# Kernel optimization log

Measured on AMD Instinct MI355X. Metric: run time of the kernel, lower is better.

The kernel has to match this reference:

```python
import jax, jax.numpy as jnp
import numpy as np

EPS = 1e-5
SLOPE = 0.01  # torch LeakyReLU default

def _conv(x, w, b, stride):
    # x: [B,C,L], w: [O,I,3]
    y = jax.lax.conv_general_dilated(x, w, (stride,), [(1, 1)],
                                     dimension_numbers=("NCH", "OIH", "NCH"))
    return y + b[None, :, None]

def _bn(x, g, b, m, v):
    # eval-mode BatchNorm1d with running stats
    inv = jax.lax.rsqrt(v + EPS)
    return (x - m[None, :, None]) * (g * inv)[None, :, None] + b[None, :, None]

def _lrelu(x):
    return jnp.where(x >= 0, x, SLOPE * x)

def setup_inputs() -> dict:
    key = jax.random.key(0)
    ks = jax.random.split(key, 32)
    B, C, L = 32, 256, 2048
    K, D = 4096, 128
    d = {}
    d["x"] = jax.random.normal(ks[0], (B, C, L), dtype=jnp.float32)
    # conv weights [O,I,3]
    d["w1"] = jax.random.normal(ks[1], (256, 256, 3), jnp.float32) * 0.03
    d["b1"] = jax.random.normal(ks[2], (256,), jnp.float32) * 0.01
    d["w2"] = jax.random.normal(ks[3], (512, 256, 3), jnp.float32) * 0.03
    d["b2"] = jax.random.normal(ks[4], (512,), jnp.float32) * 0.01
    d["w3"] = jax.random.normal(ks[5], (512, 512, 3), jnp.float32) * 0.02
    d["b3"] = jax.random.normal(ks[6], (512,), jnp.float32) * 0.01
    d["w4"] = jax.random.normal(ks[7], (D, 512, 3), jnp.float32) * 0.02
    d["b4"] = jax.random.normal(ks[8], (D,), jnp.float32) * 0.01
    for i, ch in enumerate([256, 512, 512, D]):
        d[f"g{i+1}"] = 1.0 + 0.1 * jax.random.normal(ks[9 + 4 * i], (ch,), jnp.float32)
        d[f"be{i+1}"] = 0.1 * jax.random.normal(ks[10 + 4 * i], (ch,), jnp.float32)
        d[f"m{i+1}"] = 0.1 * jax.random.normal(ks[11 + 4 * i], (ch,), jnp.float32)
        d[f"v{i+1}"] = 0.5 + jax.random.uniform(ks[12 + 4 * i], (ch,), jnp.float32)
    d["emb"] = jax.random.uniform(ks[30], (K, D), jnp.float32,
                                  minval=-1.0 / K, maxval=1.0 / K)
    return d

def reference(x, w1, b1, w2, b2, w3, b3, w4, b4,
              g1, be1, m1, v1, g2, be2, m2, v2,
              g3, be3, m3, v3, g4, be4, m4, v4, emb):
    h = _lrelu(_bn(_conv(x, w1, b1, 2), g1, be1, m1, v1))   # [B,256,L/2]
    h = _lrelu(_bn(_conv(h, w2, b2, 2), g2, be2, m2, v2))   # [B,512,L/4]
    h = _lrelu(_bn(_conv(h, w3, b3, 2), g3, be3, m3, v3))   # [B,512,L/8]
    h = _lrelu(_bn(_conv(h, w4, b4, 1), g4, be4, m4, v4))   # [B,D,L/8]
    flat = jnp.transpose(h, (0, 2, 1)).reshape(-1, h.shape[1])  # [N,D]
    # squared-distance expansion: ||f||^2 + ||e||^2 - 2 f.e
    dist = (jnp.sum(flat * flat, axis=1, keepdims=True)
            + jnp.sum(emb * emb, axis=1)
            - 2.0 * flat @ emb.T)                            # [N,K]
    codes = jnp.argmin(dist, axis=1)
    return codes, dist
```

## Files before the change

### kernel.cpp

```cpp
#include <hip/hip_runtime.h>
#include <cstdint>
#include <math.h>

#define EPS_BN 1e-5f
#define SLOPE 0.01f
#define C14 6.103515625e-5f
#define SC14 16384.0f
#define HMIN 6.103515625e-5f

typedef __attribute__((ext_vector_type(8))) _Float16 half8;
typedef __attribute__((ext_vector_type(8))) short short8;
typedef __attribute__((ext_vector_type(16))) float f32x16;
typedef __attribute__((ext_vector_type(4))) float f32x4;

__device__ __forceinline__ void split16(float v, unsigned short& uh,
                                        unsigned short& ul) {
    _Float16 h = (_Float16)v;
    if (fabsf(v) < HMIN) h = (_Float16)0.0f;
    float rem = v - (float)h;
    _Float16 l = (_Float16)(rem * SC14);
    uh = __builtin_bit_cast(unsigned short, h);
    ul = __builtin_bit_cast(unsigned short, l);
}

typedef const __attribute__((address_space(1))) unsigned int* gas_ptr;
typedef __attribute__((address_space(3))) unsigned int* las_ptr;
__device__ __forceinline__ void glds16(const void* g, void* l) {
    __builtin_amdgcn_global_load_lds((gas_ptr)g, (las_ptr)l, 16, 0, 0);
}

__global__ __launch_bounds__(256)
void wprep_all(const float* __restrict__ w1, short* __restrict__ o1,
               const float* __restrict__ w2, short* __restrict__ o2,
               const float* __restrict__ w3, short* __restrict__ o3,
               const float* __restrict__ w4, short* __restrict__ o4)
{
    const float* w; short* wbuf; int CIN, COUT;
    switch (blockIdx.y) {
        case 0: w = w1; wbuf = o1; CIN = 256; COUT = 256; break;
        case 1: w = w2; wbuf = o2; CIN = 256; COUT = 512; break;
        case 2: w = w3; wbuf = o3; CIN = 512; COUT = 512; break;
        default: w = w4; wbuf = o4; CIN = 512; COUT = 128; break;
    }
    int KST = CIN / 16, OB = COUT / 128;
    int total = KST * OB * 1536;
    for (int sid = blockIdx.x * 256 + threadIdx.x; sid < total;
         sid += gridDim.x * 256) {
        int slot = sid % 1536;
        int kb = sid / 1536;
        int ob = kb % OB, ks = kb / OB;
        int m = slot & 31, hi = (slot >> 5) & 1, mf = (slot >> 6) & 3;
        int ts = slot >> 8;
        int t = ts >> 1, s = ts & 1;
        int oc = ob * 128 + mf * 32 + m;
        int ib = ks * 16 + hi * 8;
        short8 r;
        #pragma unroll
        for (int j = 0; j < 8; ++j) {
            float v = w[((size_t)oc * CIN + ib + j) * 3 + t];
            unsigned short uh, ul;
            split16(v, uh, ul);
            r[j] = (short)(s == 0 ? uh : ul);
        }
        *(short8*)(wbuf + (size_t)sid * 8) = r;
    }
}

__global__ __launch_bounds__(256)
void bnprep_init(
    const float* __restrict__ g1, const float* __restrict__ be1,
    const float* __restrict__ m1, const float* __restrict__ v1,
    const float* __restrict__ b1, float* __restrict__ sc1, float* __restrict__ off1,
    const float* __restrict__ g2, const float* __restrict__ be2,
    const float* __restrict__ m2, const float* __restrict__ v2,
    const float* __restrict__ b2, float* __restrict__ sc2, float* __restrict__ off2,
    const float* __restrict__ g3, const float* __restrict__ be3,
    const float* __restrict__ m3, const float* __restrict__ v3,
    const float* __restrict__ b3, float* __restrict__ sc3, float* __restrict__ off3,
    const float* __restrict__ g4, const float* __restrict__ be4,
    const float* __restrict__ m4, const float* __restrict__ v4,
    const float* __restrict__ b4, float* __restrict__ sc4, float* __restrict__ off4,
    unsigned long long* __restrict__ mp)
{
    int bid = blockIdx.x;
    if (bid >= 6) {
        mp[(bid - 6) * 256 + threadIdx.x] = ~0ULL;
        return;
    }
    const float *g, *be, *m, *v, *bias;
    float *sc, *off;
    int c;
    if (bid == 0) {
        g = g1; be = be1; m = m1; v = v1; bias = b1; sc = sc1; off = off1;
        c = threadIdx.x;
    } else if (bid <= 2) {
        g = g2; be = be2; m = m2; v = v2; bias = b2; sc = sc2; off = off2;
        c = (bid - 1) * 256 + threadIdx.x;
    } else if (bid <= 4) {
        g = g3; be = be3; m = m3; v = v3; bias = b3; sc = sc3; off = off3;
        c = (bid - 3) * 256 + threadIdx.x;
    } else {
        g = g4; be = be4; m = m4; v = v4; bias = b4; sc = sc4; off = off4;
        c = threadIdx.x;
        if (c >= 128) return;
    }
    float s = g[c] / sqrtf(v[c] + EPS_BN);
    sc[c] = s;
    off[c] = (bias[c] - m[c]) * s + be[c];
}

__global__ __launch_bounds__(256)
void xsplit(const float* __restrict__ x, short* __restrict__ xpl)
{
    const size_t PL = (size_t)32 * 32 * 2 * 1025 * 8;
    int l = blockIdx.x * 256 + threadIdx.x;
    int g = blockIdx.y, b = blockIdx.z;
    float v[8];
    #pragma unroll
    for (int j = 0; j < 8; ++j)
        v[j] = x[((size_t)b * 256 + g * 8 + j) * 2048 + l];
    int arr = l & 1;
    int slot = arr ? (l + 1) / 2 : l / 2 + 1;
    size_t base = ((((size_t)b * 32 + g) * 2 + arr) * 1025 + slot) * 8;
    short8 rh, rl;
    #pragma unroll
    for (int j = 0; j < 8; ++j) {
        unsigned short uh, ul;
        split16(v[j], uh, ul);
        rh[j] = (short)uh; rl[j] = (short)ul;
    }
    *(short8*)(xpl + base) = rh;
    *(short8*)(xpl + PL + base) = rl;
    if (l == 0) {
        short8 z;
        #pragma unroll
        for (int j = 0; j < 8; ++j) z[j] = 0;
        for (int sg = 0; sg < 2; ++sg)
            for (int a2 = 0; a2 < 2; ++a2)
                *(short8*)(xpl + sg * PL +
                           ((((size_t)b * 32 + g) * 2 + a2) * 1025) * 8) = z;
    }
}

template<int CIN, int COUT, int LIN, int TILE, int EPI>
__global__ __launch_bounds__(512, 1)
void conv_pair(const short* __restrict__ wbuf, const short* __restrict__ xpl,
               const float* __restrict__ scv, const float* __restrict__ offv,
               short* __restrict__ opl)
{
    constexpr int LOUT = LIN / 2;
    constexpr int KST = CIN / 16;
    constexpr int OBS = COUT / 128;
    constexpr int NG = CIN / 8;
    constexpr int SLOTS = LIN / 2 + 1;
    constexpr size_t PLIN = (size_t)32 * NG * 2 * SLOTS * 8;
    constexpr int NF = TILE / 64;
    constexpr int NGo = COUT / 8;
    constexpr int OSLOTS = (EPI == 0) ? (LOUT / 2 + 1) : (LOUT + 2);
    constexpr size_t PLOUT = (size_t)32 * NGo * ((EPI == 0) ? 2 : 1) * OSLOTS * 8;

    constexpr int XOFF = 49152;
    constexpr int SCOFF = 69632;
    __shared__ __align__(16) char lds[71680];

    const int tid = threadIdx.x;
    const int lane = tid & 63;
    const int wv = tid >> 6;
    const int wo = wv >> 2;
    const int wm = (wv >> 1) & 1, wn = wv & 1;
    const int hi = lane >> 5, n32 = lane & 31;
    const int n0 = blockIdx.x * TILE;
    const int oby = blockIdx.y;
    const int o0 = oby * 256;
    const int b = blockIdx.z;

    if (tid < 256) ((float*)(lds + SCOFF))[tid] = scv[o0 + tid];
    else ((float*)(lds + SCOFF + 1024))[tid - 256] = offv[o0 + tid - 256];

    f32x16 acc0[2][2], acc1[2][2];
    #pragma unroll
    for (int i = 0; i < 2; ++i)
        #pragma unroll
        for (int j = 0; j < 2; ++j)
            #pragma unroll
            for (int e = 0; e < 16; ++e) { acc0[i][j][e] = 0.0f; acc1[i][j][e] = 0.0f; }

    #pragma unroll 1
    for (int ks = 0; ks < KST; ++ks) {
        __syncthreads();
        {
            const short* wsrc = wbuf +
                ((size_t)ks * OBS + (oby * 2 + wo)) * 1536 * 8;
            #pragma unroll
            for (int it = 0; it < 6; ++it) {
                int slot0 = it * 256 + (wv & 3) * 64;
                glds16(wsrc + (size_t)(slot0 + lane) * 8,
                       lds + wo * 24576 + slot0 * 16);
            }
        }
        {
            int g0 = ks * 2;
            int r = wv;
            int sg = r >> 2, rhi = (r >> 1) & 1, arr = r & 1;
            int start = arr ? n0 : (n0 + 1);
            int cnt = arr ? (TILE + 1) : TILE;
            const short* src = xpl + (size_t)sg * PLIN
                + ((((size_t)b * NG + (g0 + rhi)) * 2 + arr) * SLOTS + start) * 8;
            char* dst = lds + XOFF + ((sg * 2 + rhi) * 2 + arr) * 2112;
            for (int c0 = 0; c0 < cnt; c0 += 64) {
                if (lane < cnt - c0)
                    glds16(src + (size_t)(c0 + lane) * 8, dst + c0 * 16);
            }
        }
        __syncthreads();
        #pragma unroll
        for (int t = 0; t < 3; ++t) {
            half8 af[2][2], bx[2][2];
            #pragma unroll
            for (int s = 0; s < 2; ++s) {
                #pragma unroll
                for (int mf = 0; mf < 2; ++mf)
                    af[s][mf] = *(const half8*)(lds + wo * 24576 +
                        (((t * 2 + s) * 4 + (wm * 2 + mf)) * 64 + lane) * 16);
                int arr = (t == 1) ? 0 : 1;
                int tof = (t == 2) ? 1 : 0;
                #pragma unroll
                for (int nf = 0; nf < NF; ++nf) {
                    int qb = wn * (TILE / 2) + nf * 32 + tof;
                    bx[s][nf] = *(const half8*)(lds + XOFF + s * 8448
                                                + arr * 2112 + qb * 16
                                                + hi * 4224 + n32 * 16);
                }
            }
            #pragma unroll
            for (int mf = 0; mf < 2; ++mf)
                #pragma unroll
                for (int nf = 0; nf < NF; ++nf) {
                    acc0[mf][nf] = __builtin_amdgcn_mfma_f32_32x32x16_f16(
                        af[0][mf], bx[0][nf], acc0[mf][nf], 0, 0, 0);
                    acc1[mf][nf] = __builtin_amdgcn_mfma_f32_32x32x16_f16(
                        af[0][mf], bx[1][nf], acc1[mf][nf], 0, 0, 0);
                    acc1[mf][nf] = __builtin_amdgcn_mfma_f32_32x32x16_f16(
                        af[1][mf], bx[0][nf], acc1[mf][nf], 0, 0, 0);
                }
        }
    }

    #pragma unroll
    for (int half = 0; half < NF; ++half) {
        __syncthreads();
        #pragma unroll
        for (int mf = 0; mf < 2; ++mf)
            #pragma unroll
            for (int r = 0; r < 16; ++r) {
                int ocl = mf * 32 + (r & 3) + 8 * (r >> 2) + 4 * hi;
                *(float*)(lds + wv * 8704 + n32 * 272 + ocl * 4) =
                    acc0[mf][half][r] + C14 * acc1[mf][half][r];
            }
        __syncthreads();
        #pragma unroll
        for (int it = 0; it < 4; ++it) {
            int sl = tid + it * 512;
            int w = sl >> 8, rem = sl & 255, p = rem >> 3, grp = rem & 7;
            int wo_ = w >> 2, wm_ = (w >> 1) & 1, wn_ = w & 1;
            f32x4 v0 = *(f32x4*)(lds + w * 8704 + p * 272 + grp * 32);
            f32x4 v1 = *(f32x4*)(lds + w * 8704 + p * 272 + grp * 32 + 16);
            int ocb = wo_ * 128 + wm_ * 64 + grp * 8;
            f32x4 s0 = *(f32x4*)(lds + SCOFF + ocb * 4);
            f32x4 s1 = *(f32x4*)(lds + SCOFF + ocb * 4 + 16);
            f32x4 q0 = *(f32x4*)(lds + SCOFF + 1024 + ocb * 4);
            f32x4 q1 = *(f32x4*)(lds + SCOFF + 1024 + ocb * 4 + 16);
            float y[8];
            #pragma unroll
            for (int j = 0; j < 4; ++j) {
                float a = v0[j] * s0[j] + q0[j];
                y[j] = a >= 0.0f ? a : SLOPE * a;
                float c = v1[j] * s1[j] + q1[j];
                y[4 + j] = c >= 0.0f ? c : SLOPE * c;
            }
            int pos_abs = n0 + wn_ * (TILE / 2) + half * 32 + p;
            int oc_abs = o0 + ocb;
            short8 rh, rl;
            #pragma unroll
            for (int j = 0; j < 8; ++j) {
                unsigned short uh, ul;
                split16(y[j], uh, ul);
                rh[j] = (short)uh; rl[j] = (short)ul;
            }
            int gq = oc_abs >> 3;
            size_t base;
            if (EPI == 0) {
                int arr = pos_abs & 1;
                int slot = arr ? (pos_abs + 1) / 2 : pos_abs / 2 + 1;
                base = ((((size_t)b * NGo + gq) * 2 + arr) * OSLOTS + slot) * 8;
            } else {
                base = (((size_t)b * NGo + gq) * OSLOTS + (pos_abs + 1)) * 8;
            }
            *(short8*)(opl + base) = rh;
            *(short8*)(opl + PLOUT + base) = rl;
        }
    }

    if (EPI == 0) {
        if (blockIdx.x == 0 && tid < 128) {
            int sg = tid >> 6, r2 = tid & 63, g16 = r2 >> 1, a2 = r2 & 1;
            int gq = oby * 32 + g16;
            short8 z;
            #pragma unroll
            for (int j = 0; j < 8; ++j) z[j] = 0;
            *(short8*)(opl + (size_t)sg * PLOUT +
                       ((((size_t)b * NGo + gq) * 2 + a2) * OSLOTS) * 8) = z;
        }
    } else {
        if (tid < 64 && (blockIdx.x == 0 || blockIdx.x == gridDim.x - 1)) {
            int sg = tid >> 5, g16 = tid & 31;
            int gq = oby * 32 + g16;
            int slot = (blockIdx.x == 0) ? 0 : (OSLOTS - 1);
            short8 z;
            #pragma unroll
            for (int j = 0; j < 8; ++j) z[j] = 0;
            *(short8*)(opl + (size_t)sg * PLOUT +
                       (((size_t)b * NGo + gq) * OSLOTS + slot) * 8) = z;
        }
    }
}

template<int CIN, int COUT, int LIN>
__global__ __launch_bounds__(256, 2)
void conv_s1(const short* __restrict__ wbuf, const short* __restrict__ xpl,
             const float* __restrict__ scv, const float* __restrict__ offv,
             float* __restrict__ fout)
{
    constexpr int KST = CIN / 16;
    constexpr int OB = COUT / 128;
    constexpr int NG = CIN / 8;
    constexpr int SLOTS = LIN + 2;
    constexpr size_t PLIN = (size_t)32 * NG * SLOTS * 8;

    constexpr int XOFF = 24576;
    constexpr int BUF  = 41472;
    constexpr int SCOFF = BUF;
    __shared__ __align__(16) char lds[BUF + 1024];

    const int tid = threadIdx.x;
    const int lane = tid & 63;
    const int wv = tid >> 6;
    const int wm = wv >> 1, wn = wv & 1;
    const int hi = lane >> 5, n32 = lane & 31;
    const int n0 = blockIdx.x * 128;
    const int ob = blockIdx.y;
    const int o0 = ob * 128;
    const int b = blockIdx.z;

    if (tid < 128) {
        ((float*)(lds + SCOFF))[tid] = scv[o0 + tid];
        ((float*)(lds + SCOFF + 512))[tid] = offv[o0 + tid];
    }

    f32x16 acc0[2][2], acc1[2][2];
    #pragma unroll
    for (int i = 0; i < 2; ++i)
        #pragma unroll
        for (int j = 0; j < 2; ++j)
            #pragma unroll
            for (int e = 0; e < 16; ++e) { acc0[i][j][e] = 0.0f; acc1[i][j][e] = 0.0f; }

    const short* wg = wbuf + (size_t)ob * 1536 * 8;
    const int lanexoff = hi * 4224 + n32 * 16;

    #pragma unroll 1
    for (int ks = 0; ks < KST; ++ks) {
        __syncthreads();
        {
            const short* wsrc = wg + (size_t)ks * OB * 1536 * 8;
            #pragma unroll
            for (int it = 0; it < 6; ++it) {
                int slot0 = it * 256 + wv * 64;
                glds16(wsrc + (size_t)(slot0 + lane) * 8, lds + slot0 * 16);
            }
        }
        {
            int g0 = ks * 2;
            for (int r = wv; r < 4; r += 4) {
                int sg = r >> 1, rhi = r & 1;
                const short* src = xpl + (size_t)sg * PLIN
                    + (((size_t)b * NG + (g0 + rhi)) * SLOTS + n0) * 8;
                char* dst = lds + XOFF + (sg * 2 + rhi) * 2112;
                for (int c0 = 0; c0 < 130; c0 += 64) {
                    if (lane < 130 - c0)
                        glds16(src + (size_t)(c0 + lane) * 8, dst + c0 * 16);
                }
            }
        }
        __syncthreads();
        #pragma unroll
        for (int t = 0; t < 3; ++t) {
            half8 af[2][2], bx[2][2];
            #pragma unroll
            for (int s = 0; s < 2; ++s) {
                #pragma unroll
                for (int mf = 0; mf < 2; ++mf)
                    af[s][mf] = *(const half8*)(lds +
                        (((t * 2 + s) * 4 + (wm * 2 + mf)) * 64 + lane) * 16);
                #pragma unroll
                for (int nf = 0; nf < 2; ++nf) {
                    int qb = wn * 64 + nf * 32 + t;
                    bx[s][nf] = *(const half8*)(lds + XOFF + s * 4224
                                                + qb * 16 + hi * 2112 + n32 * 16);
                }
            }
            #pragma unroll
            for (int mf = 0; mf < 2; ++mf)
                #pragma unroll
                for (int nf = 0; nf < 2; ++nf) {
                    acc0[mf][nf] = __builtin_amdgcn_mfma_f32_32x32x16_f16(
                        af[0][mf], bx[0][nf], acc0[mf][nf], 0, 0, 0);
                    acc1[mf][nf] = __builtin_amdgcn_mfma_f32_32x32x16_f16(
                        af[0][mf], bx[1][nf], acc1[mf][nf], 0, 0, 0);
                    acc1[mf][nf] = __builtin_amdgcn_mfma_f32_32x32x16_f16(
                        af[1][mf], bx[0][nf], acc1[mf][nf], 0, 0, 0);
                }
        }
    }

    #pragma unroll
    for (int half = 0; half < 2; ++half) {
        __syncthreads();
        #pragma unroll
        for (int mf = 0; mf < 2; ++mf)
            #pragma unroll
            for (int r = 0; r < 16; ++r) {
                int ocl = mf * 32 + (r & 3) + 8 * (r >> 2) + 4 * hi;
                *(float*)(lds + wv * 8704 + n32 * 272 + ocl * 4) =
                    acc0[mf][half][r] + C14 * acc1[mf][half][r];
            }
        __syncthreads();
        #pragma unroll
        for (int it = 0; it < 4; ++it) {
            int sl = tid + it * 256;
            int w = sl >> 8, rem = sl & 255, p = rem >> 3, grp = rem & 7;
            int wm_ = w >> 1, wn_ = w & 1;
            f32x4 v0 = *(f32x4*)(lds + w * 8704 + p * 272 + grp * 32);
            f32x4 v1 = *(f32x4*)(lds + w * 8704 + p * 272 + grp * 32 + 16);
            int oclb = wm_ * 64 + grp * 8;
            f32x4 s0 = *(f32x4*)(lds + SCOFF + oclb * 4);
            f32x4 s1 = *(f32x4*)(lds + SCOFF + oclb * 4 + 16);
            f32x4 q0 = *(f32x4*)(lds + SCOFF + 512 + oclb * 4);
            f32x4 q1 = *(f32x4*)(lds + SCOFF + 512 + oclb * 4 + 16);
            f32x4 w0, w1;
            #pragma unroll
            for (int j = 0; j < 4; ++j) {
                float a = v0[j] * s0[j] + q0[j];
                w0[j] = a >= 0.0f ? a : SLOPE * a;
                float c = v1[j] * s1[j] + q1[j];
                w1[j] = c >= 0.0f ? c : SLOPE * c;
            }
            int pos_abs = n0 + wn_ * 64 + half * 32 + p;
            float* fp = fout + ((size_t)(b * 256 + pos_abs)) * 128 + o0 + oclb;
            *(f32x4*)fp = w0;
            *(f32x4*)(fp + 4) = w1;
        }
    }
}

__global__ __launch_bounds__(256)
void split_kernel(const float* __restrict__ src, int nrows,
                  short* __restrict__ ph, short* __restrict__ pl,
                  float* __restrict__ sumv)
{
    int t = blockIdx.x * 256 + threadIdx.x;
    int n = t >> 4, g = t & 15;
    if (n >= nrows) return;
    const float* rowp = src + (size_t)n * 128 + g * 8;
    float4 v0 = *(const float4*)rowp;
    float4 v1 = *(const float4*)(rowp + 4);
    float vv[8] = {v0.x, v0.y, v0.z, v0.w, v1.x, v1.y, v1.z, v1.w};
    short8 rh, rl;
    float ss = 0.0f;
    #pragma unroll
    for (int j = 0; j < 8; ++j) {
        float v = vv[j];
        ss = fmaf(v, v, ss);
        unsigned short uh, ul;
        split16(v, uh, ul);
        rh[j] = (short)uh; rl[j] = (short)ul;
    }
    int nb = n >> 5, m = n & 31, ks = g >> 1, hi = g & 1;
    size_t slot = ((((size_t)nb * 8 + ks) * 2 + hi) * 32 + m) * 8;
    *(short8*)(ph + slot) = rh;
    *(short8*)(pl + slot) = rl;
    #pragma unroll
    for (int mk = 8; mk; mk >>= 1) ss += __shfl_xor(ss, mk);
    if (g == 0) sumv[n] = ss;
}

__global__ __launch_bounds__(256, 2)
void distmin_kernel(const short* __restrict__ fh, const short* __restrict__ fl,
                    const short* __restrict__ eh, const short* __restrict__ el,
                    const float* __restrict__ sf, const float* __restrict__ se,
                    float* __restrict__ dist, unsigned long long* __restrict__ mp)
{
    __shared__ unsigned long long cand[128 * 64];
    const int tid = threadIdx.x;
    const int lane = tid & 63;
    const int wv = tid >> 6;
    const int wm = wv >> 1, wn = wv & 1;
    const int hi = lane >> 5, n32 = lane & 31;
    const int kb = blockIdx.x;
    const int nb = blockIdx.y;

    f32x16 acc0[2][2], acc1[2][2];
    #pragma unroll
    for (int i = 0; i < 2; ++i)
        #pragma unroll
        for (int j = 0; j < 2; ++j)
            #pragma unroll
            for (int e = 0; e < 16; ++e) { acc0[i][j][e] = 0.0f; acc1[i][j][e] = 0.0f; }

    const short* fb[2][2];
    const short* eb[2][2];
    {
        const short* fpl[2] = {fh, fl};
        const short* epl[2] = {eh, el};
        #pragma unroll
        for (int s = 0; s < 2; ++s) {
            #pragma unroll
            for (int mf = 0; mf < 2; ++mf)
                fb[s][mf] = fpl[s] + (size_t)nb * 16384
                            + ((size_t)(wm * 2 + mf) * 8 * 64 + lane) * 8;
            #pragma unroll
            for (int nf = 0; nf < 2; ++nf)
                eb[s][nf] = epl[s]
                            + ((size_t)(kb * 4 + wn * 2 + nf) * 8 * 64 + lane) * 8;
        }
    }

    #pragma unroll
    for (int ks = 0; ks < 8; ++ks) {
        half8 af[2][2], bx[2][2];
        #pragma unroll
        for (int s = 0; s < 2; ++s) {
            #pragma unroll
            for (int mf = 0; mf < 2; ++mf)
                af[s][mf] = *(const half8*)(fb[s][mf] + ks * 512);
            #pragma unroll
            for (int nf = 0; nf < 2; ++nf)
                bx[s][nf] = *(const half8*)(eb[s][nf] + ks * 512);
        }
        #pragma unroll
        for (int mf = 0; mf < 2; ++mf)
            #pragma unroll
            for (int nf = 0; nf < 2; ++nf) {
                acc0[mf][nf] = __builtin_amdgcn_mfma_f32_32x32x16_f16(
                    af[0][mf], bx[0][nf], acc0[mf][nf], 0, 0, 0);
                acc1[mf][nf] = __builtin_amdgcn_mfma_f32_32x32x16_f16(
                    af[0][mf], bx[1][nf], acc1[mf][nf], 0, 0, 0);
                acc1[mf][nf] = __builtin_amdgcn_mfma_f32_32x32x16_f16(
                    af[1][mf], bx[0][nf], acc1[mf][nf], 0, 0, 0);
            }
    }

    const int n_blk = nb * 128;
    const int kc0 = kb * 128 + wn * 64 + n32;
    const float se0 = se[kc0];
    const float se1 = se[kc0 + 32];
    #pragma unroll
    for (int mf = 0; mf < 2; ++mf) {
        #pragma unroll
        for (int r = 0; r < 16; ++r) {
            int nloc = wm * 64 + mf * 32 + (r & 3) + 8 * (r >> 2) + 4 * hi;
            int n = n_blk + nloc;
            float sfn = sf[n];
            float d0 = acc0[mf][0][r] + C14 * acc1[mf][0][r];
            float d1 = acc0[mf][1][r] + C14 * acc1[mf][1][r];
            float v0 = (sfn + se0) - 2.0f * d0;
            float v1 = (sfn + se1) - 2.0f * d1;
            __builtin_nontemporal_store(v0, &dist[(size_t)n * 4096 + kc0]);
            __builtin_nontemporal_store(v1, &dist[(size_t)n * 4096 + kc0 + 32]);
            unsigned long long p0 =
                (((unsigned long long)__float_as_uint(v0)) << 32) | (unsigned)kc0;
            unsigned long long p1 =
                (((unsigned long long)__float_as_uint(v1)) << 32) | (unsigned)(kc0 + 32);
            unsigned long long p = p1 < p0 ? p1 : p0;
            cand[nloc * 64 + wn * 32 + n32] = p;
        }
    }
    __syncthreads();
    {
        int row = tid >> 1, h = tid & 1;
        unsigned long long best = ~0ULL;
        #pragma unroll
        for (int i = 0; i < 32; ++i) {
            int c = h * 32 + ((i + row) & 31);
            unsigned long long cv = cand[row * 64 + c];
            best = cv < best ? cv : best;
        }
        unsigned lo = (unsigned)best, hw = (unsigned)(best >> 32);
        unsigned lo2 = __shfl_xor(lo, 1), hw2 = __shfl_xor(hw, 1);
        unsigned long long ob = (((unsigned long long)hw2) << 32) | lo2;
        if (ob < best) best = ob;
        if (h == 0) atomicMin(mp + n_blk + row, best);
    }
}

__global__ __launch_bounds__(256)
void codes_kernel(const unsigned long long* __restrict__ mp,
                  float* __restrict__ codes)
{
    int n = blockIdx.x * 256 + threadIdx.x;
    if (n < 8192) codes[n] = (float)(unsigned)(mp[n] & 0xffffffffULL);
}

extern "C" void kernel_launch(void* const* d_in, const int* in_sizes, int n_in,
                              void* d_out, int out_size, void* d_ws, size_t ws_size,
                              hipStream_t stream)
{
    const float* x   = (const float*)d_in[0];
    const float* w1  = (const float*)d_in[1];
    const float* b1  = (const float*)d_in[2];
    const float* w2  = (const float*)d_in[3];
    const float* b2  = (const float*)d_in[4];
    const float* w3  = (const float*)d_in[5];
    const float* b3  = (const float*)d_in[6];
    const float* w4  = (const float*)d_in[7];
    const float* b4  = (const float*)d_in[8];
    const float* g1  = (const float*)d_in[9];
    const float* be1 = (const float*)d_in[10];
    const float* m1  = (const float*)d_in[11];
    const float* v1  = (const float*)d_in[12];
    const float* g2  = (const float*)d_in[13];
    const float* be2 = (const float*)d_in[14];
    const float* m2  = (const float*)d_in[15];
    const float* v2  = (const float*)d_in[16];
    const float* g3  = (const float*)d_in[17];
    const float* be3 = (const float*)d_in[18];
    const float* m3  = (const float*)d_in[19];
    const float* v3  = (const float*)d_in[20];
    const float* g4  = (const float*)d_in[21];
    const float* be4 = (const float*)d_in[22];
    const float* m4  = (const float*)d_in[23];
    const float* v4  = (const float*)d_in[24];
    const float* emb = (const float*)d_in[25];

    float* outf  = (float*)d_out;
    float* codes = outf;
    float* distm = outf + 8192;

    char* wsb = (char*)d_ws;
    short* wb1 = (short*)(wsb + 0);
    short* wb2 = (short*)(wsb + 786432);
    short* wb3 = (short*)(wsb + 2359296);
    short* wb4 = (short*)(wsb + 5505024);
    float* sc1 = (float*)(wsb + 6291456); float* off1 = sc1 + 256;
    float* sc2 = (float*)(wsb + 6293504); float* off2 = sc2 + 512;
    float* sc3 = (float*)(wsb + 6297600); float* off3 = sc3 + 512;
    float* sc4 = (float*)(wsb + 6301696); float* off4 = sc4 + 128;
    short* h1p = (short*)(wsb + 6302720);
    short* fh  = (short*)(wsb + 39922688);
    short* fl  = (short*)(wsb + 42019840);
    short* eh  = (short*)(wsb + 44116992);
    short* el  = (short*)(wsb + 45165568);
    float* sf  = (float*)(wsb + 46214144);
    float* se  = (float*)(wsb + 46246912);
    unsigned long long* mp = (unsigned long long*)(wsb + 46263296);

    char* db = (char*)distm;
    short* xpl = (short*)db;
    short* h2p = (short*)db;
    short* h3p = (short*)(db + 33685504);
    float* f   = (float*)(db + 80000000);

    wprep_all<<<dim3(192, 4), 256, 0, stream>>>(w1, wb1, w2, wb2, w3, wb3, w4, wb4);
    bnprep_init<<<38, 256, 0, stream>>>(
        g1, be1, m1, v1, b1, sc1, off1,
        g2, be2, m2, v2, b2, sc2, off2,
        g3, be3, m3, v3, b3, sc3, off3,
        g4, be4, m4, v4, b4, sc4, off4, mp);
    split_kernel<<<256, 256, 0, stream>>>(emb, 4096, eh, el, se);

    xsplit<<<dim3(8, 32, 32), 256, 0, stream>>>(x, xpl);
    conv_pair<256, 256, 2048, 128, 0>
        <<<dim3(8, 1, 32), 512, 0, stream>>>(wb1, xpl, sc1, off1, h1p);
    conv_pair<256, 512, 1024, 128, 0>
        <<<dim3(4, 2, 32), 512, 0, stream>>>(wb2, h1p, sc2, off2, h2p);
    conv_pair<512, 512, 512, 64, 1>
        <<<dim3(4, 2, 32), 512, 0, stream>>>(wb3, h2p, sc3, off3, h3p);
    conv_s1<512, 128, 256>
        <<<dim3(2, 1, 32), 256, 0, stream>>>(wb4, h3p, sc4, off4, f);

    split_kernel<<<512, 256, 0, stream>>>(f, 8192, fh, fl, sf);
    distmin_kernel<<<dim3(32, 64), 256, 0, stream>>>(fh, fl, eh, el,
                                                     sf, se, distm, mp);
    codes_kernel<<<32, 256, 0, stream>>>(mp, codes);
}
```

Before: 263.8 us.

## Double-buffer conv LDS staging and fuse feature split into final conv epilogue

Both conv kernels now keep two LDS buffers and issue the global-to-LDS loads for the next K step before computing the current one. They wait with explicit vmcnt counts and raw barriers, and raise wave priority around the MFMA block, so load latency overlaps compute. The last conv's epilogue now writes the fp16 hi/lo split features and atomically accumulates squared norms directly, removing the fp32 feature buffer and a separate split kernel launch. This costs twice the LDS per block and relies on hand-counted vmcnt values that must match the number of issued loads; the atomic norm accumulation also changes summation order.

```diff
diff --git a/kernel.cpp b/kernel.cpp
--- a/kernel.cpp
+++ b/kernel.cpp
@@ -27,6 +27,18 @@
 typedef __attribute__((address_space(3))) unsigned int* las_ptr;
 __device__ __forceinline__ void glds16(const void* g, void* l) {
     __builtin_amdgcn_global_load_lds((gas_ptr)g, (las_ptr)l, 16, 0, 0);
+}
+
+template<int N>
+__device__ __forceinline__ void vm_wait() {
+    if constexpr (N == 0)      asm volatile("s_waitcnt vmcnt(0)" ::: "memory");
+    else if constexpr (N == 8) asm volatile("s_waitcnt vmcnt(8)" ::: "memory");
+    else if constexpr (N == 9) asm volatile("s_waitcnt vmcnt(9)" ::: "memory");
+}
+__device__ __forceinline__ void raw_bar() {
+    asm volatile("" ::: "memory");
+    __builtin_amdgcn_s_barrier();
+    asm volatile("" ::: "memory");
 }
 
 __global__ __launch_bounds__(256)
@@ -80,13 +92,11 @@
     const float* __restrict__ g4, const float* __restrict__ be4,
     const float* __restrict__ m4, const float* __restrict__ v4,
     const float* __restrict__ b4, float* __restrict__ sc4, float* __restrict__ off4,
-    unsigned long long* __restrict__ mp)
+    unsigned long long* __restrict__ mp, float* __restrict__ sf)
 {
     int bid = blockIdx.x;
-    if (bid >= 6) {
-        mp[(bid - 6) * 256 + threadIdx.x] = ~0ULL;
-        return;
-    }
+    if (bid >= 38) { sf[(bid - 38) * 256 + threadIdx.x] = 0.0f; return; }
+    if (bid >= 6) { mp[(bid - 6) * 256 + threadIdx.x] = ~0ULL; return; }
     const float *g, *be, *m, *v, *bias;
     float *sc, *off;
     int c;
@@ -160,8 +170,10 @@
     constexpr size_t PLOUT = (size_t)32 * NGo * ((EPI == 0) ? 2 : 1) * OSLOTS * 8;
 
     constexpr int XOFF = 49152;
-    constexpr int SCOFF = 69632;
-    __shared__ __align__(16) char lds[71680];
+    constexpr int BUF  = XOFF + 8 * 2112;
+    constexpr int SCOFF = 2 * BUF;
+    constexpr int SCNT = (TILE == 128) ? 9 : 8;
+    __shared__ __align__(16) char lds[2 * BUF + 2048];
 
     const int tid = threadIdx.x;
     const int lane = tid & 63;
@@ -185,34 +197,45 @@
             #pragma unroll
             for (int e = 0; e < 16; ++e) { acc0[i][j][e] = 0.0f; acc1[i][j][e] = 0.0f; }
 
+    auto stage = [&](char* base, int ks) {
+        const short* wsrc = wbuf + ((size_t)ks * OBS + (oby * 2 + wo)) * 1536 * 8;
+        #pragma unroll
+        for (int it = 0; it < 6; ++it) {
+            int slot0 = it * 256 + (wv & 3) * 64;
+            glds16(wsrc + (size_t)(slot0 + lane) * 8, base + wo * 24576 + slot0 * 16);
+        }
+        int g0 = ks * 2;
+        int sg = wv >> 2, rhi = (wv >> 1) & 1, arr = wv & 1;
+        int start = arr ? n0 : (n0 + 1);
+        const short* src = xpl + (size_t)sg * PLIN
+            + ((((size_t)b * NG + (g0 + rhi)) * 2 + arr) * SLOTS + start) * 8;
+        char* dst = base + XOFF + ((sg * 2 + rhi) * 2 + arr) * 2112;
+        if (TILE == 128) {
+            glds16(src + (size_t)lane * 8, dst);
+            glds16(src + (size_t)(64 + lane) * 8, dst + 64 * 16);
+            int c2 = arr ? 65 : 64;
+            glds16(src + (size_t)(c2 + lane) * 8, dst + c2 * 16);
+        } else {
+            glds16(src + (size_t)lane * 8, dst);
+            int c1 = arr ? 1 : 0;
+            glds16(src + (size_t)(c1 + lane) * 8, dst + c1 * 16);
+        }
+    };
+
+    stage(lds, 0);
+
     #pragma unroll 1
     for (int ks = 0; ks < KST; ++ks) {
-        __syncthreads();
-        {
-            const short* wsrc = wbuf +
-                ((size_t)ks * OBS + (oby * 2 + wo)) * 1536 * 8;
-            #pragma unroll
-            for (int it = 0; it < 6; ++it) {
-                int slot0 = it * 256 + (wv & 3) * 64;
-                glds16(wsrc + (size_t)(slot0 + lane) * 8,
-                       lds + wo * 24576 + slot0 * 16);
-            }
-        }
-        {
-            int g0 = ks * 2;
-            int r = wv;
-            int sg = r >> 2, rhi = (r >> 1) & 1, arr = r & 1;
-            int start = arr ? n0 : (n0 + 1);
-            int cnt = arr ? (TILE + 1) : TILE;
-            const short* src = xpl + (size_t)sg * PLIN
-                + ((((size_t)b * NG + (g0 + rhi)) * 2 + arr) * SLOTS + start) * 8;
-            char* dst = lds + XOFF + ((sg * 2 + rhi) * 2 + arr) * 2112;
-            for (int c0 = 0; c0 < cnt; c0 += 64) {
-                if (lane < cnt - c0)
-                    glds16(src + (size_t)(c0 + lane) * 8, dst + c0 * 16);
-            }
-        }
-        __syncthreads();
+        char* cbase = lds + (ks & 1) * BUF;
+        char* nbase = lds + ((ks & 1) ^ 1) * BUF;
+        if (ks + 1 < KST) {
+            stage(nbase, ks + 1);
+            vm_wait<SCNT>();
+        } else {
+            vm_wait<0>();
+        }
+        raw_bar();
+        __builtin_amdgcn_s_setprio(1);
         #pragma unroll
         for (int t = 0; t < 3; ++t) {
             half8 af[2][2], bx[2][2];
@@ -220,14 +243,14 @@
             for (int s = 0; s < 2; ++s) {
                 #pragma unroll
                 for (int mf = 0; mf < 2; ++mf)
-                    af[s][mf] = *(const half8*)(lds + wo * 24576 +
+                    af[s][mf] = *(const half8*)(cbase + wo * 24576 +
                         (((t * 2 + s) * 4 + (wm * 2 + mf)) * 64 + lane) * 16);
                 int arr = (t == 1) ? 0 : 1;
                 int tof = (t == 2) ? 1 : 0;
                 #pragma unroll
                 for (int nf = 0; nf < NF; ++nf) {
                     int qb = wn * (TILE / 2) + nf * 32 + tof;
-                    bx[s][nf] = *(const half8*)(lds + XOFF + s * 8448
+                    bx[s][nf] = *(const half8*)(cbase + XOFF + s * 8448
                                                 + arr * 2112 + qb * 16
                                                 + hi * 4224 + n32 * 16);
                 }
@@ -244,6 +267,8 @@
                         af[1][mf], bx[0][nf], acc1[mf][nf], 0, 0, 0);
                 }
         }
+        __builtin_amdgcn_s_setprio(0);
+        raw_bar();
     }
 
     #pragma unroll
@@ -329,18 +354,18 @@
 __global__ __launch_bounds__(256, 2)
 void conv_s1(const short* __restrict__ wbuf, const short* __restrict__ xpl,
              const float* __restrict__ scv, const float* __restrict__ offv,
-             float* __restrict__ fout)
+             short* __restrict__ fh, short* __restrict__ fl,
+             float* __restrict__ sf)
 {
     constexpr int KST = CIN / 16;
-    constexpr int OB = COUT / 128;
     constexpr int NG = CIN / 8;
     constexpr int SLOTS = LIN + 2;
     constexpr size_t PLIN = (size_t)32 * NG * SLOTS * 8;
 
     constexpr int XOFF = 24576;
-    constexpr int BUF  = 41472;
-    constexpr int SCOFF = BUF;
-    __shared__ __align__(16) char lds[BUF + 1024];
+    constexpr int BUF  = XOFF + 4 * 2112;
+    constexpr int SCOFF = 2 * BUF;
+    __shared__ __align__(16) char lds[2 * BUF + 1024];
 
     const int tid = threadIdx.x;
     const int lane = tid & 63;
@@ -348,13 +373,11 @@
     const int wm = wv >> 1, wn = wv & 1;
     const int hi = lane >> 5, n32 = lane & 31;
     const int n0 = blockIdx.x * 128;
-    const int ob = blockIdx.y;
-    const int o0 = ob * 128;
     const int b = blockIdx.z;
 
     if (tid < 128) {
-        ((float*)(lds + SCOFF))[tid] = scv[o0 + tid];
-        ((float*)(lds + SCOFF + 512))[tid] = offv[o0 + tid];
+        ((float*)(lds + SCOFF))[tid] = scv[tid];
+        ((float*)(lds + SCOFF + 512))[tid] = offv[tid];
     }
 
     f32x16 acc0[2][2], acc1[2][2];
@@ -365,34 +388,37 @@
             #pragma unroll
             for (int e = 0; e < 16; ++e) { acc0[i][j][e] = 0.0f; acc1[i][j][e] = 0.0f; }
 
-    const short* wg = wbuf + (size_t)ob * 1536 * 8;
-    const int lanexoff = hi * 4224 + n32 * 16;
+    auto stage = [&](char* base, int ks) {
+        const short* wsrc = wbuf + (size_t)ks * 1536 * 8;
+        #pragma unroll
+        for (int it = 0; it < 6; ++it) {
+            int slot0 = it * 256 + wv * 64;
+            glds16(wsrc + (size_t)(slot0 + lane) * 8, base + slot0 * 16);
+        }
+        int g0 = ks * 2;
+        int sg = wv >> 1, rhi = wv & 1;
+        const short* src = xpl + (size_t)sg * PLIN
+            + (((size_t)b * NG + (g0 + rhi)) * SLOTS + n0) * 8;
+        char* dst = base + XOFF + (sg * 2 + rhi) * 2112;
+        glds16(src + (size_t)lane * 8, dst);
+        glds16(src + (size_t)(64 + lane) * 8, dst + 64 * 16);
+        glds16(src + (size_t)(66 + lane) * 8, dst + 66 * 16);
+    };
+
+    stage(lds, 0);
 
     #pragma unroll 1
     for (int ks = 0; ks < KST; ++ks) {
-        __syncthreads();
-        {
-            const short* wsrc = wg + (size_t)ks * OB * 1536 * 8;
-            #pragma unroll
-            for (int it = 0; it < 6; ++it) {
-                int slot0 = it * 256 + wv * 64;
-                glds16(wsrc + (size_t)(slot0 + lane) * 8, lds + slot0 * 16);
-            }
-        }
-        {
-            int g0 = ks * 2;
-            for (int r = wv; r < 4; r += 4) {
-                int sg = r >> 1, rhi = r & 1;
-                const short* src = xpl + (size_t)sg * PLIN
-                    + (((size_t)b * NG + (g0 + rhi)) * SLOTS + n0) * 8;
-                char* dst = lds + XOFF + (sg * 2 + rhi) * 2112;
-                for (int c0 = 0; c0 < 130; c0 += 64) {
-                    if (lane < 130 - c0)
-                        glds16(src + (size_t)(c0 + lane) * 8, dst + c0 * 16);
-                }
-            }
-        }
-        __syncthreads();
+        char* cbase = lds + (ks & 1) * BUF;
+        char* nbase = lds + ((ks & 1) ^ 1) * BUF;
+        if (ks + 1 < KST) {
+            stage(nbase, ks + 1);
+            vm_wait<9>();
+        } else {
+            vm_wait<0>();
+        }
+        raw_bar();
+        __builtin_amdgcn_s_setprio(1);
         #pragma unroll
         for (int t = 0; t < 3; ++t) {
             half8 af[2][2], bx[2][2];
@@ -400,12 +426,12 @@
             for (int s = 0; s < 2; ++s) {
                 #pragma unroll
                 for (int mf = 0; mf < 2; ++mf)
-                    af[s][mf] = *(const half8*)(lds +
+                    af[s][mf] = *(const half8*)(cbase +
                         (((t * 2 + s) * 4 + (wm * 2 + mf)) * 64 + lane) * 16);
                 #pragma unroll
                 for (int nf = 0; nf < 2; ++nf) {
                     int qb = wn * 64 + nf * 32 + t;
-                    bx[s][nf] = *(const half8*)(lds + XOFF + s * 4224
+                    bx[s][nf] = *(const half8*)(cbase + XOFF + s * 4224
                                                 + qb * 16 + hi * 2112 + n32 * 16);
                 }
             }
@@ -421,6 +447,8 @@
                         af[1][mf], bx[0][nf], acc1[mf][nf], 0, 0, 0);
                 }
         }
+        __builtin_amdgcn_s_setprio(0);
+        raw_bar();
     }
 
     #pragma unroll
@@ -447,18 +475,31 @@
             f32x4 s1 = *(f32x4*)(lds + SCOFF + oclb * 4 + 16);
             f32x4 q0 = *(f32x4*)(lds + SCOFF + 512 + oclb * 4);
             f32x4 q1 = *(f32x4*)(lds + SCOFF + 512 + oclb * 4 + 16);
-            f32x4 w0, w1;
+            float y[8];
             #pragma unroll
             for (int j = 0; j < 4; ++j) {
                 float a = v0[j] * s0[j] + q0[j];
-                w0[j] = a >= 0.0f ? a : SLOPE * a;
+                y[j] = a >= 0.0f ? a : SLOPE * a;
                 float c = v1[j] * s1[j] + q1[j];
-                w1[j] = c >= 0.0f ? c : SLOPE * c;
+                y[4 + j] = c >= 0.0f ? c : SLOPE * c;
             }
             int pos_abs = n0 + wn_ * 64 + half * 32 + p;
-            float* fp = fout + ((size_t)(b * 256 + pos_abs)) * 128 + o0 + oclb;
-            *(f32x4*)fp = w0;
-            *(f32x4*)(fp + 4) = w1;
+            int n = b * 256 + pos_abs;
+            short8 rh, rl;
+            float partial = 0.0f;
+            #pragma unroll
+            for (int j = 0; j < 8; ++j) {
+                partial = fmaf(y[j], y[j], partial);
+                unsigned short uh, ul;
+                split16(y[j], uh, ul);
+                rh[j] = (short)uh; rl[j] = (short)ul;
+            }
+            int g = wm_ * 8 + grp;
+            size_t slot = ((((size_t)(n >> 5) * 8 + (g >> 1)) * 2 + (g & 1)) * 32
+                           + (n & 31)) * 8;
+            *(short8*)(fh + slot) = rh;
+            *(short8*)(fl + slot) = rl;
+            atomicAdd(sf + n, partial);
         }
     }
 }
@@ -668,14 +709,13 @@
     short* xpl = (short*)db;
     short* h2p = (short*)db;
     short* h3p = (short*)(db + 33685504);
-    float* f   = (float*)(db + 80000000);
 
     wprep_all<<<dim3(192, 4), 256, 0, stream>>>(w1, wb1, w2, wb2, w3, wb3, w4, wb4);
-    bnprep_init<<<38, 256, 0, stream>>>(
+    bnprep_init<<<70, 256, 0, stream>>>(
         g1, be1, m1, v1, b1, sc1, off1,
         g2, be2, m2, v2, b2, sc2, off2,
         g3, be3, m3, v3, b3, sc3, off3,
-        g4, be4, m4, v4, b4, sc4, off4, mp);
+        g4, be4, m4, v4, b4, sc4, off4, mp, sf);
     split_kernel<<<256, 256, 0, stream>>>(emb, 4096, eh, el, se);
 
     xsplit<<<dim3(8, 32, 32), 256, 0, stream>>>(x, xpl);
@@ -686,9 +726,8 @@
     conv_pair<512, 512, 512, 64, 1>
         <<<dim3(4, 2, 32), 512, 0, stream>>>(wb3, h2p, sc3, off3, h3p);
     conv_s1<512, 128, 256>
-        <<<dim3(2, 1, 32), 256, 0, stream>>>(wb4, h3p, sc4, off4, f);
-
-    split_kernel<<<512, 256, 0, stream>>>(f, 8192, fh, fl, sf);
+        <<<dim3(2, 1, 32), 256, 0, stream>>>(wb4, h3p, sc4, off4, fh, fl, sf);
+
     distmin_kernel<<<dim3(32, 64), 256, 0, stream>>>(fh, fl, eh, el,
                                                      sf, se, distm, mp);
     codes_kernel<<<32, 256, 0, stream>>>(mp, codes);
```

Measured after the change: 261.4 us. Within noise of the previous version (-0.9%).
